# Performance work log

Hardware: AMD Instinct MI355X
Metric: run time of the kernel (lower is better)

## Reference

```python
import jax, jax.numpy as jnp
import numpy as np

B, N, START = 16, 16, 2048
D, H, HK, DH, CTX = 4096, 32, 8, 128, 4096
T = START + N
REP = H // HK
ROPE_THETA = 500000.0


def setup_inputs() -> dict:
    key = jax.random.key(0)
    ks = jax.random.split(key, 8)
    x = jax.random.normal(ks[0], (B, N, D), jnp.float32)
    # rotary frequencies for absolute positions START..T-1
    half = DH // 2
    inv_freq = 1.0 / (ROPE_THETA ** (np.arange(half, dtype=np.float64) * 2.0 / DH))
    pos = np.arange(START, T, dtype=np.float64)
    ang = pos[:, None] * inv_freq[None, :]  # (N, DH//2)
    freqs_cos = jnp.asarray(np.cos(ang), jnp.float32)
    freqs_sin = jnp.asarray(np.sin(ang), jnp.float32)
    # causal additive mask: query i (abs pos START+i) may attend to key j <= START+i
    i = np.arange(N)[:, None]
    j = np.arange(T)[None, :]
    mask = np.where(j <= START + i, 0.0, -1e9).astype(np.float32)
    mask = jnp.asarray(mask)[None, None]  # (1,1,N,T)
    cache_k = jax.random.normal(ks[1], (B, HK, CTX, DH), jnp.float32)
    cache_v = jax.random.normal(ks[2], (B, HK, CTX, DH), jnp.float32)
    s = 0.02
    wq = jax.random.normal(ks[3], (D, H * DH), jnp.float32) * s
    wk = jax.random.normal(ks[4], (D, HK * DH), jnp.float32) * s
    wv = jax.random.normal(ks[5], (D, HK * DH), jnp.float32) * s
    wo = jax.random.normal(ks[6], (D, D), jnp.float32) * s
    return {"x": x, "freqs_cos": freqs_cos, "freqs_sin": freqs_sin, "mask": mask,
            "cache_k": cache_k, "cache_v": cache_v,
            "wq": wq, "wk": wk, "wv": wv, "wo": wo, "start_pos": START}


def _rope(t, cos, sin):
    # t: (B, N, h, DH); cos/sin: (N, DH//2) -> broadcast (1, N, 1, DH//2)
    tr = t.reshape(*t.shape[:-1], -1, 2)
    a, b = tr[..., 0], tr[..., 1]
    c = cos[None, :, None, :]
    s = sin[None, :, None, :]
    out = jnp.stack([a * c - b * s, a * s + b * c], axis=-1)
    return out.reshape(t.shape)


def reference(x, freqs_cos, freqs_sin, mask, cache_k, cache_v, wq, wk, wv, wo, start_pos):
    Bx, Nx, _ = x.shape
    t_end = start_pos + Nx
    xq = (x @ wq).reshape(Bx, Nx, H, DH)
    xk = (x @ wk).reshape(Bx, Nx, HK, DH)
    xv = (x @ wv).reshape(Bx, Nx, HK, DH)
    xq = _rope(xq, freqs_cos, freqs_sin)
    xk = _rope(xk, freqs_cos, freqs_sin)
    xq = xq.transpose(0, 2, 1, 3)  # (B,H,N,DH)
    xk = xk.transpose(0, 2, 1, 3)  # (B,HK,N,DH)
    xv = xv.transpose(0, 2, 1, 3)
    # KV-cache scatter update, then slice to current length
    cache_k = cache_k.at[:, :, start_pos:t_end].set(xk)
    cache_v = cache_v.at[:, :, start_pos:t_end].set(xv)
    k = cache_k[:, :, :t_end]  # (B,HK,T,DH)
    v = cache_v[:, :, :t_end]
    # GQA masked SDPA
    q = xq.reshape(Bx, HK, REP, Nx, DH)
    scale = 1.0 / jnp.sqrt(jnp.float32(DH))
    scores = jnp.einsum('bkrnd,bktd->bkrnt', q, k) * scale
    scores = scores + mask[:, :, None]  # (1,1,1,N,T) broadcast
    p = jax.nn.softmax(scores, axis=-1)
    z = jnp.einsum('bkrnt,bktd->bkrnd', p, v)
    z = z.reshape(Bx, H, Nx, DH).transpose(0, 2, 1, 3).reshape(Bx, Nx, D)
    return z @ wo
```

## Files before the change

### kernel.cpp

```cpp
#include <hip/hip_runtime.h>


#define CTX 4096

typedef __attribute__((ext_vector_type(8))) short short8;
typedef __attribute__((ext_vector_type(4))) float f32x4;

__device__ __forceinline__ unsigned short f2bf(float f) {
  union { float f; unsigned u; } a; a.f = f;
  unsigned r = a.u + 0x7FFFu + ((a.u >> 16) & 1u);
  return (unsigned short)(r >> 16);
}

__device__ __forceinline__ f32x4 mfma_bf16(short8 a, short8 b, f32x4 c) {
  return __builtin_amdgcn_mfma_f32_16x16x32_bf16(a, b, c, 0, 0, 0);
}

__device__ __forceinline__ void gll16(const unsigned short* g, unsigned short* l) {
  __builtin_amdgcn_global_load_lds(
      (__attribute__((address_space(1))) unsigned int*)(g),
      (__attribute__((address_space(3))) unsigned int*)(l), 16, 0, 0);
}

__global__ __launch_bounds__(256) void k_prep(const float* __restrict__ wq,
    const float* __restrict__ wk, const float* __restrict__ wv,
    const float* __restrict__ wo, const float* __restrict__ x,
    unsigned short* __restrict__ wqkvT, unsigned short* __restrict__ woT,
    unsigned short* __restrict__ xb)
{
  const int bid = blockIdx.x, tid = threadIdx.x;
  if (bid >= 10240) {
    int e4 = (bid - 10240) * 256 + tid;
    float4 v = ((const float4*)x)[e4];
    ushort4 o; o.x = f2bf(v.x); o.y = f2bf(v.y); o.z = f2bf(v.z); o.w = f2bf(v.w);
    ((ushort4*)xb)[e4] = o;
    return;
  }
  __shared__ unsigned short Ts[64][66];
  const float* src; unsigned short* dst; int N; int t = bid;
  if (t < 4096)      {            src = wq; dst = wqkvT;                        N = 4096; }
  else if (t < 5120) { t -= 4096; src = wk; dst = wqkvT + (size_t)4096 * 4096;  N = 1024; }
  else if (t < 6144) { t -= 5120; src = wv; dst = wqkvT + (size_t)5120 * 4096;  N = 1024; }
  else               { t -= 6144; src = wo; dst = woT;                          N = 4096; }
  const int kt = t & 63, bn = t >> 6;
  const int k0 = kt * 64, n0 = bn * 64;
#pragma unroll
  for (int i = 0; i < 4; ++i) {
    int u = tid + i * 256;
    int k = u >> 4, n4 = u & 15;
    float4 v = *(const float4*)(src + (size_t)(k0 + k) * N + n0 + n4 * 4);
    Ts[k][n4 * 4 + 0] = f2bf(v.x); Ts[k][n4 * 4 + 1] = f2bf(v.y);
    Ts[k][n4 * 4 + 2] = f2bf(v.z); Ts[k][n4 * 4 + 3] = f2bf(v.w);
  }
  __syncthreads();
  {
    int nn = tid >> 2, seg = tid & 3;
    unsigned short v[16];
#pragma unroll
    for (int j = 0; j < 16; ++j) v[j] = Ts[seg * 16 + j][nn];
    unsigned short* d = dst + (size_t)(n0 + nn) * 4096 + k0 + seg * 16;
    *(short8*)d       = *(const short8*)&v[0];
    *(short8*)(d + 8) = *(const short8*)&v[8];
  }
}

__global__ __launch_bounds__(256) void k_gemm(const unsigned short* __restrict__ A,
    const unsigned short* __restrict__ BT, float* __restrict__ Cp, int Ntot)
{
  __shared__ unsigned short sA[128 * 64];
  __shared__ unsigned short sB[64 * 64];
  const int tid = threadIdx.x;
  const int w = tid >> 6, lane = tid & 63, quad = lane >> 4, l16 = lane & 15;
  const int wm = (w & 1) << 6, wn = (w >> 1) << 5;
  const int bn = blockIdx.x, bm = blockIdx.y, ks = blockIdx.z;
  const int r8 = lane >> 3, c8 = (lane & 7) << 3;

  const unsigned short* Ab = A + (size_t)(bm * 128) * 4096 + (ks << 10);
  const unsigned short* Bb = BT + (size_t)(bn * 64) * 4096 + (ks << 10);

  f32x4 acc[4][2];
#pragma unroll
  for (int mf = 0; mf < 4; ++mf)
#pragma unroll
    for (int nf = 0; nf < 2; ++nf) acc[mf][nf] = (f32x4){0.f, 0.f, 0.f, 0.f};

  for (int kt = 0; kt < 16; ++kt) {
#pragma unroll
    for (int i = 0; i < 4; ++i)
      gll16(Ab + (size_t)(w * 32 + i * 8 + r8) * 4096 + kt * 64 + c8,
            &sA[(w * 32 + i * 8) * 64]);
#pragma unroll
    for (int i = 0; i < 2; ++i)
      gll16(Bb + (size_t)(w * 16 + i * 8 + r8) * 4096 + kt * 64 + c8,
            &sB[(w * 16 + i * 8) * 64]);
    __syncthreads();
#pragma unroll
    for (int kk = 0; kk < 2; ++kk) {
      short8 af[4], bfr[2];
#pragma unroll
      for (int mf = 0; mf < 4; ++mf)
        af[mf] = *(const short8*)&sA[(wm + mf * 16 + l16) * 64 + kk * 32 + quad * 8];
#pragma unroll
      for (int nf = 0; nf < 2; ++nf)
        bfr[nf] = *(const short8*)&sB[(wn + nf * 16 + l16) * 64 + kk * 32 + quad * 8];
#pragma unroll
      for (int mf = 0; mf < 4; ++mf)
#pragma unroll
        for (int nf = 0; nf < 2; ++nf)
          acc[mf][nf] = mfma_bf16(af[mf], bfr[nf], acc[mf][nf]);
    }
    __syncthreads();
  }

  float* Cz = Cp + (size_t)ks * 256 * Ntot;
#pragma unroll
  for (int mf = 0; mf < 4; ++mf)
#pragma unroll
    for (int nf = 0; nf < 2; ++nf)
#pragma unroll
      for (int r = 0; r < 4; ++r)
        Cz[(size_t)(bm * 128 + wm + mf * 16 + quad * 4 + r) * Ntot
           + bn * 64 + wn + nf * 16 + l16] = acc[mf][nf][r];
}

__global__ __launch_bounds__(256) void k_kvfin(const float* __restrict__ qp,
    const float* __restrict__ fcos, const float* __restrict__ fsin,
    float* __restrict__ ck, float* __restrict__ cv, unsigned short* __restrict__ qbf)
{
  const float scale = 0.08838834764831845f;
  const size_t PS = (size_t)256 * 6144;
  int id = blockIdx.x * 256 + threadIdx.x;
  if (id < 524288) {
    int m = id >> 11, pc = id & 2047;
    int h = pc >> 6, fi = pc & 63, npos = m & 15;
    size_t off = (size_t)m * 6144 + h * 128 + 2 * fi;
    float a = 0.f, b2 = 0.f;
#pragma unroll
    for (int s = 0; s < 4; ++s) { a += qp[s * PS + off]; b2 += qp[s * PS + off + 1]; }
    float c = fcos[npos * 64 + fi], sn = fsin[npos * 64 + fi];
    unsigned short o0 = f2bf((a * c - b2 * sn) * scale);
    unsigned short o1 = f2bf((a * sn + b2 * c) * scale);
    qbf[(size_t)m * 4096 + h * 128 + 2 * fi]     = o0;
    qbf[(size_t)m * 4096 + h * 128 + 2 * fi + 1] = o1;
  } else if (id < 655360) {
    int e = id - 524288;
    int m = e >> 9, pc = e & 511;
    int hk = pc >> 6, fi = pc & 63;
    int b = m >> 4, npos = m & 15;
    size_t off = (size_t)m * 6144 + 4096 + hk * 128 + 2 * fi;
    float a = 0.f, b2 = 0.f;
#pragma unroll
    for (int s = 0; s < 4; ++s) { a += qp[s * PS + off]; b2 += qp[s * PS + off + 1]; }
    float c = fcos[npos * 64 + fi], sn = fsin[npos * 64 + fi];
    float* dst = ck + ((size_t)(b * 8 + hk) * CTX + 2048 + npos) * 128 + 2 * fi;
    dst[0] = a * c - b2 * sn;
    dst[1] = a * sn + b2 * c;
  } else {
    int e = id - 655360;
    int m = e >> 10, cc = e & 1023;
    int b = m >> 4, npos = m & 15;
    int hk = cc >> 7, dh = cc & 127;
    size_t off = (size_t)m * 6144 + 5120 + cc;
    float a = 0.f;
#pragma unroll
    for (int s = 0; s < 4; ++s) a += qp[s * PS + off];
    cv[((size_t)(b * 8 + hk) * CTX + 2048 + npos) * 128 + dh] = a;
  }
}

__global__ __launch_bounds__(256) void k_attn(const unsigned short* __restrict__ qbf,
    const float* __restrict__ ck, const float* __restrict__ cv,
    unsigned short* __restrict__ zpO, float* __restrict__ zpL)
{
  __shared__ unsigned short Ks[32][136];
  __shared__ unsigned short Vs[128][34];
  __shared__ unsigned short Ps[4][16][40];

  const int tid = threadIdx.x;
  const int w = tid >> 6, lane = tid & 63, quad = lane >> 4, l16 = lane & 15;
  const int bid = blockIdx.x;
  const int split = bid & 3, hk = (bid >> 2) & 7, b = bid >> 5;
  const int h = hk * 4 + w;

  short8 qf[4];
  {
    const unsigned short* qrow = qbf + (size_t)(b * 16 + l16) * 4096 + h * 128;
#pragma unroll
    for (int kf = 0; kf < 4; ++kf)
      qf[kf] = *(const short8*)(qrow + kf * 32 + quad * 8);
  }

  const float* Kg = ck + (size_t)(b * 8 + hk) * CTX * 128;
  const float* Vg = cv + (size_t)(b * 8 + hk) * CTX * 128;
  const int tb = split * 512;
  const int NT = (split == 3) ? 17 : 16;

  f32x4 O[8];
#pragma unroll
  for (int df = 0; df < 8; ++df) O[df] = (f32x4){0.f, 0.f, 0.f, 0.f};
  float lp[4] = {0.f, 0.f, 0.f, 0.f};

  float4 pk[4], pv[4];
#define A_LOAD(IT_) do { \
    _Pragma("unroll") for (int i = 0; i < 4; ++i) { \
      int u = tid + (i << 8); int trow = u >> 5, c4 = u & 31; \
      size_t off = (size_t)(tb + (IT_) * 32 + trow) * 128 + c4 * 4; \
      pk[i] = *(const float4*)(Kg + off); \
      pv[i] = *(const float4*)(Vg + off); \
    } } while (0)
#define A_STORE() do { \
    _Pragma("unroll") for (int i = 0; i < 4; ++i) { \
      int u = tid + (i << 8); int trow = u >> 5, c4 = u & 31; \
      ushort4 k4; k4.x = f2bf(pk[i].x); k4.y = f2bf(pk[i].y); \
      k4.z = f2bf(pk[i].z); k4.w = f2bf(pk[i].w); \
      *(ushort4*)&Ks[trow][c4 * 4] = k4; \
      Vs[c4 * 4 + 0][trow] = f2bf(pv[i].x); \
      Vs[c4 * 4 + 1][trow] = f2bf(pv[i].y); \
      Vs[c4 * 4 + 2][trow] = f2bf(pv[i].z); \
      Vs[c4 * 4 + 3][trow] = f2bf(pv[i].w); \
    } } while (0)

  A_LOAD(0);
  A_STORE();
  __syncthreads();

  for (int it = 0; it < NT; ++it) {
    if (it + 1 < NT) A_LOAD(it + 1);

    f32x4 S0 = (f32x4){0.f,0.f,0.f,0.f}, S1 = (f32x4){0.f,0.f,0.f,0.f};
#pragma unroll
    for (int kf = 0; kf < 4; ++kf) {
      short8 k0 = *(const short8*)&Ks[l16][kf * 32 + quad * 8];
      short8 k1 = *(const short8*)&Ks[16 + l16][kf * 32 + quad * 8];
      S0 = mfma_bf16(qf[kf], k0, S0);
      S1 = mfma_bf16(qf[kf], k1, S1);
    }

    const bool lastT = (split == 3) && (it == 16);
    float p0[4], p1[4];
#pragma unroll
    for (int r = 0; r < 4; ++r) {
      int row = quad * 4 + r;
      if (!lastT) { p0[r] = __expf(S0[r]); p1[r] = __expf(S1[r]); }
      else        { p0[r] = (l16 <= row) ? __expf(S0[r]) : 0.f; p1[r] = 0.f; }
      lp[r] += p0[r] + p1[r];
      Ps[w][row][l16]      = f2bf(p0[r]);
      Ps[w][row][16 + l16] = f2bf(p1[r]);
    }

    short8 pf = *(const short8*)&Ps[w][l16][quad * 8];
#pragma unroll
    for (int df = 0; df < 8; ++df) {
      short8 vb = *(const short8*)&Vs[df * 16 + l16][quad * 8];
      O[df] = mfma_bf16(pf, vb, O[df]);
    }

    __syncthreads();
    if (it + 1 < NT) A_STORE();
    __syncthreads();
  }
#undef A_LOAD
#undef A_STORE

#pragma unroll
  for (int r = 0; r < 4; ++r)
#pragma unroll
    for (int off = 1; off < 16; off <<= 1) lp[r] += __shfl_xor(lp[r], off);

#pragma unroll
  for (int df = 0; df < 8; ++df)
#pragma unroll
    for (int r = 0; r < 4; ++r)
      zpO[(size_t)(split * 256 + b * 16 + quad * 4 + r) * 4096 + h * 128 + df * 16 + l16]
          = f2bf(O[df][r]);

  if (l16 == 0) {
#pragma unroll
    for (int r = 0; r < 4; ++r)
      zpL[((split * 16 + b) * 32 + h) * 16 + quad * 4 + r] = lp[r];
  }
}

__global__ __launch_bounds__(256) void k_combine(const unsigned short* __restrict__ zpO,
    const float* __restrict__ zpL, unsigned short* __restrict__ zb)
{
  int e = blockIdx.x * 256 + threadIdx.x;
  int m = e >> 12, col = e & 4095;
  int b = m >> 4, npos = m & 15, h = col >> 7;
  float num = 0.f, den = 0.f;
#pragma unroll
  for (int s = 0; s < 4; ++s) {
    union { unsigned u; float f; } cv2;
    cv2.u = (unsigned)zpO[(size_t)s * 1048576 + e] << 16;
    num += cv2.f;
    den += zpL[((s * 16 + b) * 32 + h) * 16 + npos];
  }
  zb[e] = f2bf(num / den);
}

__global__ __launch_bounds__(256) void k_fin(const float* __restrict__ op,
                                             float* __restrict__ out)
{
  int e4 = blockIdx.x * 256 + threadIdx.x;
  float4 o = ((const float4*)op)[e4];
#pragma unroll
  for (int s = 1; s < 4; ++s) {
    float4 p = ((const float4*)(op + (size_t)s * 1048576))[e4];
    o.x += p.x; o.y += p.y; o.z += p.z; o.w += p.w;
  }
  ((float4*)out)[e4] = o;
}

extern "C" void kernel_launch(void* const* d_in, const int* in_sizes, int n_in,
                              void* d_out, int out_size, void* d_ws, size_t ws_size,
                              hipStream_t stream) {
  const float* x  = (const float*)d_in[0];
  const float* fc = (const float*)d_in[1];
  const float* fs = (const float*)d_in[2];
  float* ck = (float*)d_in[4];
  float* cv = (float*)d_in[5];
  const float* wq = (const float*)d_in[6];
  const float* wk = (const float*)d_in[7];
  const float* wv = (const float*)d_in[8];
  const float* wo = (const float*)d_in[9];
  float* out = (float*)d_out;

  char* ws = (char*)d_ws;
#define MB(x) ((size_t)(x) << 20)
  unsigned short* xb    = (unsigned short*)(ws);
  unsigned short* wqkvT = (unsigned short*)(ws + MB(2));
  unsigned short* woT   = (unsigned short*)(ws + MB(50));
  float*          qpart = (float*)(ws + MB(82));
  unsigned short* zb    = (unsigned short*)(ws + MB(108));
  unsigned short* zpO   = (unsigned short*)(ws + MB(110));
  float*          zpL   = (float*)(ws + MB(118));
  float*          opart = (float*)(ws + MB(119));
  unsigned short* qbf   = (unsigned short*)(ws + MB(136));
#undef MB

  k_prep<<<11264, 256, 0, stream>>>(wq, wk, wv, wo, x, wqkvT, woT, xb);
  k_gemm<<<dim3(96, 2, 4), 256, 0, stream>>>(xb, wqkvT, qpart, 6144);
  k_kvfin<<<3584, 256, 0, stream>>>(qpart, fc, fs, ck, cv, qbf);
  k_attn<<<512, 256, 0, stream>>>(qbf, ck, cv, zpO, zpL);
  k_combine<<<4096, 256, 0, stream>>>(zpO, zpL, zb);
  k_gemm<<<dim3(64, 2, 4), 256, 0, stream>>>(zb, woT, opart, 4096);
  k_fin<<<1024, 256, 0, stream>>>(opart, out);
}
```

Measured before the change: 652.4 us.

## Fuse fp32 weight conversion into GEMM B-tile loads, drop separate transpose pass

Removes the k_prep pass that converted and transposed all weights to bf16 in a workspace. The GEMM now reads fp32 weights directly, converts them to bf16 and transposes them into LDS as it loads each tile. Each block now covers all 256 rows of M, so every weight element is read only once. The attention kernel also changes its V loads so that each thread stores four consecutive tokens as one vector, instead of doing four scalar transposed LDS writes. The trade-off is that weight loads become strided scalar fp32 reads and the GEMM launches fewer, larger blocks.

```diff
diff --git a/kernel.cpp b/kernel.cpp
--- a/kernel.cpp
+++ b/kernel.cpp
@@ -22,105 +22,85 @@
       (__attribute__((address_space(3))) unsigned int*)(l), 16, 0, 0);
 }
 
-__global__ __launch_bounds__(256) void k_prep(const float* __restrict__ wq,
-    const float* __restrict__ wk, const float* __restrict__ wv,
-    const float* __restrict__ wo, const float* __restrict__ x,
-    unsigned short* __restrict__ wqkvT, unsigned short* __restrict__ woT,
-    unsigned short* __restrict__ xb)
-{
-  const int bid = blockIdx.x, tid = threadIdx.x;
-  if (bid >= 10240) {
-    int e4 = (bid - 10240) * 256 + tid;
-    float4 v = ((const float4*)x)[e4];
-    ushort4 o; o.x = f2bf(v.x); o.y = f2bf(v.y); o.z = f2bf(v.z); o.w = f2bf(v.w);
-    ((ushort4*)xb)[e4] = o;
-    return;
-  }
-  __shared__ unsigned short Ts[64][66];
-  const float* src; unsigned short* dst; int N; int t = bid;
-  if (t < 4096)      {            src = wq; dst = wqkvT;                        N = 4096; }
-  else if (t < 5120) { t -= 4096; src = wk; dst = wqkvT + (size_t)4096 * 4096;  N = 1024; }
-  else if (t < 6144) { t -= 5120; src = wv; dst = wqkvT + (size_t)5120 * 4096;  N = 1024; }
-  else               { t -= 6144; src = wo; dst = woT;                          N = 4096; }
-  const int kt = t & 63, bn = t >> 6;
-  const int k0 = kt * 64, n0 = bn * 64;
-#pragma unroll
-  for (int i = 0; i < 4; ++i) {
-    int u = tid + i * 256;
-    int k = u >> 4, n4 = u & 15;
-    float4 v = *(const float4*)(src + (size_t)(k0 + k) * N + n0 + n4 * 4);
-    Ts[k][n4 * 4 + 0] = f2bf(v.x); Ts[k][n4 * 4 + 1] = f2bf(v.y);
-    Ts[k][n4 * 4 + 2] = f2bf(v.z); Ts[k][n4 * 4 + 3] = f2bf(v.w);
-  }
-  __syncthreads();
-  {
-    int nn = tid >> 2, seg = tid & 3;
-    unsigned short v[16];
-#pragma unroll
-    for (int j = 0; j < 16; ++j) v[j] = Ts[seg * 16 + j][nn];
-    unsigned short* d = dst + (size_t)(n0 + nn) * 4096 + k0 + seg * 16;
-    *(short8*)d       = *(const short8*)&v[0];
-    *(short8*)(d + 8) = *(const short8*)&v[8];
-  }
+__global__ __launch_bounds__(256) void k_prepx(const float* __restrict__ x,
+                                               unsigned short* __restrict__ xb)
+{
+  int e4 = blockIdx.x * 256 + threadIdx.x;
+  float4 v = ((const float4*)x)[e4];
+  ushort4 o; o.x = f2bf(v.x); o.y = f2bf(v.y); o.z = f2bf(v.z); o.w = f2bf(v.w);
+  ((ushort4*)xb)[e4] = o;
 }
 
 __global__ __launch_bounds__(256) void k_gemm(const unsigned short* __restrict__ A,
-    const unsigned short* __restrict__ BT, float* __restrict__ Cp, int Ntot)
-{
-  __shared__ unsigned short sA[128 * 64];
-  __shared__ unsigned short sB[64 * 64];
+    const float* __restrict__ w0, const float* __restrict__ w1,
+    const float* __restrict__ w2, float* __restrict__ Cp, int Ntot, int qkv)
+{
+  __shared__ unsigned short sA[256 * 64];
+  __shared__ unsigned short sB[64 * 72];
   const int tid = threadIdx.x;
   const int w = tid >> 6, lane = tid & 63, quad = lane >> 4, l16 = lane & 15;
-  const int wm = (w & 1) << 6, wn = (w >> 1) << 5;
-  const int bn = blockIdx.x, bm = blockIdx.y, ks = blockIdx.z;
+  const int bn = blockIdx.x, ks = blockIdx.y;
   const int r8 = lane >> 3, c8 = (lane & 7) << 3;
 
-  const unsigned short* Ab = A + (size_t)(bm * 128) * 4096 + (ks << 10);
-  const unsigned short* Bb = BT + (size_t)(bn * 64) * 4096 + (ks << 10);
-
-  f32x4 acc[4][2];
+  const float* src; int N, nloc;
+  if (qkv && bn >= 64) {
+    if (bn < 80) { src = w1; N = 1024; nloc = (bn - 64) << 6; }
+    else         { src = w2; N = 1024; nloc = (bn - 80) << 6; }
+  } else         { src = w0; N = 4096; nloc = bn << 6; }
+
+  const unsigned short* Ab = A + (ks << 10);
+  const float* Wb = src + (size_t)(ks << 10) * N + nloc;
+  const int gn = tid & 63, gk = (tid >> 6) << 4;
+
+  f32x4 acc[4][4];
 #pragma unroll
   for (int mf = 0; mf < 4; ++mf)
 #pragma unroll
-    for (int nf = 0; nf < 2; ++nf) acc[mf][nf] = (f32x4){0.f, 0.f, 0.f, 0.f};
+    for (int nf = 0; nf < 4; ++nf) acc[mf][nf] = (f32x4){0.f, 0.f, 0.f, 0.f};
 
   for (int kt = 0; kt < 16; ++kt) {
 #pragma unroll
-    for (int i = 0; i < 4; ++i)
-      gll16(Ab + (size_t)(w * 32 + i * 8 + r8) * 4096 + kt * 64 + c8,
-            &sA[(w * 32 + i * 8) * 64]);
-#pragma unroll
-    for (int i = 0; i < 2; ++i)
-      gll16(Bb + (size_t)(w * 16 + i * 8 + r8) * 4096 + kt * 64 + c8,
-            &sB[(w * 16 + i * 8) * 64]);
+    for (int i = 0; i < 8; ++i)
+      gll16(Ab + (size_t)(w * 64 + i * 8 + r8) * 4096 + kt * 64 + c8,
+            &sA[(w * 64 + i * 8) * 64]);
+    {
+      const float* s0 = Wb + (size_t)(kt * 64 + gk) * N + gn;
+      short8 lo, hi;
+#pragma unroll
+      for (int j = 0; j < 8; ++j) lo[j] = (short)f2bf(s0[(size_t)j * N]);
+#pragma unroll
+      for (int j = 0; j < 8; ++j) hi[j] = (short)f2bf(s0[(size_t)(j + 8) * N]);
+      *(short8*)&sB[gn * 72 + gk]     = lo;
+      *(short8*)&sB[gn * 72 + gk + 8] = hi;
+    }
     __syncthreads();
 #pragma unroll
     for (int kk = 0; kk < 2; ++kk) {
-      short8 af[4], bfr[2];
+      short8 af[4], bfr[4];
 #pragma unroll
       for (int mf = 0; mf < 4; ++mf)
-        af[mf] = *(const short8*)&sA[(wm + mf * 16 + l16) * 64 + kk * 32 + quad * 8];
-#pragma unroll
-      for (int nf = 0; nf < 2; ++nf)
-        bfr[nf] = *(const short8*)&sB[(wn + nf * 16 + l16) * 64 + kk * 32 + quad * 8];
+        af[mf] = *(const short8*)&sA[(w * 64 + mf * 16 + l16) * 64 + kk * 32 + quad * 8];
+#pragma unroll
+      for (int nf = 0; nf < 4; ++nf)
+        bfr[nf] = *(const short8*)&sB[(nf * 16 + l16) * 72 + kk * 32 + quad * 8];
 #pragma unroll
       for (int mf = 0; mf < 4; ++mf)
 #pragma unroll
-        for (int nf = 0; nf < 2; ++nf)
+        for (int nf = 0; nf < 4; ++nf)
           acc[mf][nf] = mfma_bf16(af[mf], bfr[nf], acc[mf][nf]);
     }
     __syncthreads();
   }
 
-  float* Cz = Cp + (size_t)ks * 256 * Ntot;
+  float* Cz = Cp + (size_t)ks * 256 * Ntot + bn * 64;
 #pragma unroll
   for (int mf = 0; mf < 4; ++mf)
 #pragma unroll
-    for (int nf = 0; nf < 2; ++nf)
+    for (int nf = 0; nf < 4; ++nf)
 #pragma unroll
       for (int r = 0; r < 4; ++r)
-        Cz[(size_t)(bm * 128 + wm + mf * 16 + quad * 4 + r) * Ntot
-           + bn * 64 + wn + nf * 16 + l16] = acc[mf][nf][r];
+        Cz[(size_t)(w * 64 + mf * 16 + quad * 4 + r) * Ntot + nf * 16 + l16]
+            = acc[mf][nf][r];
 }
 
 __global__ __launch_bounds__(256) void k_kvfin(const float* __restrict__ qp,
@@ -173,7 +153,7 @@
     unsigned short* __restrict__ zpO, float* __restrict__ zpL)
 {
   __shared__ unsigned short Ks[32][136];
-  __shared__ unsigned short Vs[128][34];
+  __shared__ unsigned short Vs[128][36];
   __shared__ unsigned short Ps[4][16][40];
 
   const int tid = threadIdx.x;
@@ -200,13 +180,16 @@
   for (int df = 0; df < 8; ++df) O[df] = (f32x4){0.f, 0.f, 0.f, 0.f};
   float lp[4] = {0.f, 0.f, 0.f, 0.f};
 
-  float4 pk[4], pv[4];
+  float4 pk[4]; float pv[16];
 #define A_LOAD(IT_) do { \
     _Pragma("unroll") for (int i = 0; i < 4; ++i) { \
       int u = tid + (i << 8); int trow = u >> 5, c4 = u & 31; \
-      size_t off = (size_t)(tb + (IT_) * 32 + trow) * 128 + c4 * 4; \
-      pk[i] = *(const float4*)(Kg + off); \
-      pv[i] = *(const float4*)(Vg + off); \
+      pk[i] = *(const float4*)(Kg + (size_t)(tb + (IT_) * 32 + trow) * 128 + c4 * 4); \
+    } \
+    _Pragma("unroll") for (int i = 0; i < 4; ++i) { \
+      int u = tid + (i << 8); int dh = u & 127, tq = u >> 7; \
+      _Pragma("unroll") for (int j = 0; j < 4; ++j) \
+        pv[i * 4 + j] = Vg[(size_t)(tb + (IT_) * 32 + tq * 4 + j) * 128 + dh]; \
     } } while (0)
 #define A_STORE() do { \
     _Pragma("unroll") for (int i = 0; i < 4; ++i) { \
@@ -214,10 +197,12 @@
       ushort4 k4; k4.x = f2bf(pk[i].x); k4.y = f2bf(pk[i].y); \
       k4.z = f2bf(pk[i].z); k4.w = f2bf(pk[i].w); \
       *(ushort4*)&Ks[trow][c4 * 4] = k4; \
-      Vs[c4 * 4 + 0][trow] = f2bf(pv[i].x); \
-      Vs[c4 * 4 + 1][trow] = f2bf(pv[i].y); \
-      Vs[c4 * 4 + 2][trow] = f2bf(pv[i].z); \
-      Vs[c4 * 4 + 3][trow] = f2bf(pv[i].w); \
+    } \
+    _Pragma("unroll") for (int i = 0; i < 4; ++i) { \
+      int u = tid + (i << 8); int dh = u & 127, tq = u >> 7; \
+      ushort4 v4; v4.x = f2bf(pv[i * 4 + 0]); v4.y = f2bf(pv[i * 4 + 1]); \
+      v4.z = f2bf(pv[i * 4 + 2]); v4.w = f2bf(pv[i * 4 + 3]); \
+      *(ushort4*)&Vs[dh][tq * 4] = v4; \
     } } while (0)
 
   A_LOAD(0);
@@ -328,8 +313,6 @@
   char* ws = (char*)d_ws;
 #define MB(x) ((size_t)(x) << 20)
   unsigned short* xb    = (unsigned short*)(ws);
-  unsigned short* wqkvT = (unsigned short*)(ws + MB(2));
-  unsigned short* woT   = (unsigned short*)(ws + MB(50));
   float*          qpart = (float*)(ws + MB(82));
   unsigned short* zb    = (unsigned short*)(ws + MB(108));
   unsigned short* zpO   = (unsigned short*)(ws + MB(110));
@@ -338,11 +321,11 @@
   unsigned short* qbf   = (unsigned short*)(ws + MB(136));
 #undef MB
 
-  k_prep<<<11264, 256, 0, stream>>>(wq, wk, wv, wo, x, wqkvT, woT, xb);
-  k_gemm<<<dim3(96, 2, 4), 256, 0, stream>>>(xb, wqkvT, qpart, 6144);
+  k_prepx<<<1024, 256, 0, stream>>>(x, xb);
+  k_gemm<<<dim3(96, 4), 256, 0, stream>>>(xb, wq, wk, wv, qpart, 6144, 1);
   k_kvfin<<<3584, 256, 0, stream>>>(qpart, fc, fs, ck, cv, qbf);
   k_attn<<<512, 256, 0, stream>>>(qbf, ck, cv, zpO, zpL);
   k_combine<<<4096, 256, 0, stream>>>(zpO, zpL, zb);
-  k_gemm<<<dim3(64, 2, 4), 256, 0, stream>>>(zb, woT, opart, 4096);
+  k_gemm<<<dim3(64, 4), 256, 0, stream>>>(zb, wo, wo, wo, opart, 4096, 0);
   k_fin<<<1024, 256, 0, stream>>>(opart, out);
 }
```

After: 620.0 us. 1.05x faster.
